# Kernel optimization log

Hardware: AMD Instinct MI355X
Metric: run time of the kernel (lower is better)

## Reference

```python
import jax, jax.numpy as jnp
import numpy as np

EPS = 1e-7  # K.epsilon()


def setup_inputs() -> dict:
    key = jax.random.key(0)
    k1, k2, k3, k4 = jax.random.split(key, 4)
    B, T, S = 512, 32, 2048  # batch, time_steps, seq_len
    inputs = jax.random.normal(k1, (B, T, S), dtype=jnp.float32)
    # Keras mask (float 0/1), same shape as inputs
    mask = (jax.random.uniform(k2, (B, T, S)) < 0.8).astype(jnp.float32)
    # 'uniform' keras initializer: U(-0.05, 0.05)
    W = jax.random.uniform(k3, (S, T, T), minval=-0.05, maxval=0.05, dtype=jnp.float32)
    b = jax.random.uniform(k4, (S, T), minval=-0.05, maxval=0.05, dtype=jnp.float32)
    return {"inputs": inputs, "mask": mask, "W": W, "b": b}


def reference(inputs, mask, W, b):
    # (B,T,S) -> (B,S,T), apply mask
    x = jnp.transpose(inputs, (0, 2, 1)) * jnp.transpose(mask, (0, 2, 1))
    # per-position matmul, batched over B and S (replaces the tf.scan over batch)
    z = jnp.einsum('bst,stu->bsu', x, W) + b  # (B,S,T)
    e = jnp.exp(jnp.tanh(z))
    att = e / (jnp.sum(e, axis=2, keepdims=True) + EPS)  # softmax-like over T
    return jnp.sum(att * x, axis=1)  # (B,T)
```

## Files before the change

kernel.cpp:

```cpp
#include <hip/hip_runtime.h>

#define EPS_K 1e-7f

typedef __attribute__((ext_vector_type(8)))  short          frag8;
typedef __attribute__((ext_vector_type(16))) float          accf16;
typedef __attribute__((ext_vector_type(4)))  unsigned short us4;

__device__ __forceinline__ unsigned f2bf(float f) {
  union { float f; unsigned u; } v; v.f = f;
  unsigned u = v.u;
  u += 0x7FFFu + ((u >> 16) & 1u);
  return u >> 16;
}
__device__ __forceinline__ float bf2f(unsigned short s) {
  union { unsigned u; float f; } v; v.u = ((unsigned)s) << 16;
  return v.f;
}
__device__ __forceinline__ unsigned pk_bf16(float lo, float hi) {
  return f2bf(lo) | (f2bf(hi) << 16);
}

__global__ __launch_bounds__(256) void wbf_prep(
    const float* __restrict__ Wt, unsigned short* __restrict__ Wbf)
{
  __shared__ unsigned short tile[32 * 33];
  const int s   = blockIdx.x;
  const int tid = threadIdx.x;
  {
    const int t  = tid >> 3;
    const int uc = tid & 7;
    const float4 v = *(const float4*)(Wt + s * 1024 + t * 32 + 4 * uc);
    tile[t * 33 + 4 * uc + 0] = (unsigned short)f2bf(v.x);
    tile[t * 33 + 4 * uc + 1] = (unsigned short)f2bf(v.y);
    tile[t * 33 + 4 * uc + 2] = (unsigned short)f2bf(v.z);
    tile[t * 33 + 4 * uc + 3] = (unsigned short)f2bf(v.w);
  }
  __syncthreads();
  {
    const int u  = tid >> 3;
    const int tc = tid & 7;
    uint2 d;
    d.x = (unsigned)tile[(4 * tc + 0) * 33 + u] | ((unsigned)tile[(4 * tc + 1) * 33 + u] << 16);
    d.y = (unsigned)tile[(4 * tc + 2) * 33 + u] | ((unsigned)tile[(4 * tc + 3) * 33 + u] << 16);
    *(uint2*)(Wbf + s * 1024 + u * 32 + 4 * tc) = d;
  }
}

template <bool WBF>
__global__ __launch_bounds__(256, 5) void attn_fused(
    const float* __restrict__ inp,
    const float* __restrict__ msk,
    const float* __restrict__ Wt,
    const unsigned short* __restrict__ Wbf,
    const float* __restrict__ bias,
    float* __restrict__ out)
{
  __shared__ unsigned short x_us[32 * 256];

  const int tid = threadIdx.x;
  const int st  = blockIdx.x >> 4;
  const int bg  = blockIdx.x & 15;
  const int s0  = st * 8;

  {
    const int sc = tid & 1;
    const int tb = (tid >> 1) & 3;
    const int b  = tid >> 3;
    const float* ip = inp + ((size_t)(bg * 32 + b) * 32 + 8 * tb) * 2048 + s0 + 4 * sc;
    const float* mp = msk + ((size_t)(bg * 32 + b) * 32 + 8 * tb) * 2048 + s0 + 4 * sc;
    unsigned c32[4][4];
    #pragma unroll
    for (int j2 = 0; j2 < 4; ++j2) {
      const float4 vi0 = *(const float4*)(ip + (2 * j2)     * 2048);
      const float4 vm0 = *(const float4*)(mp + (2 * j2)     * 2048);
      const float4 vi1 = *(const float4*)(ip + (2 * j2 + 1) * 2048);
      const float4 vm1 = *(const float4*)(mp + (2 * j2 + 1) * 2048);
      c32[0][j2] = pk_bf16(vi0.x * vm0.x, vi1.x * vm1.x);
      c32[1][j2] = pk_bf16(vi0.y * vm0.y, vi1.y * vm1.y);
      c32[2][j2] = pk_bf16(vi0.z * vm0.z, vi1.z * vm1.z);
      c32[3][j2] = pk_bf16(vi0.w * vm0.w, vi1.w * vm1.w);
    }
    #pragma unroll
    for (int w = 0; w < 4; ++w) {
      const int L = tb * 8 + 4 * sc + w;
      unsigned* dst = (unsigned*)(x_us + b * 256 + ((L ^ (b & 7)) * 8));
      *(uint4*)dst = make_uint4(c32[w][0], c32[w][1], c32[w][2], c32[w][3]);
    }
  }
  __syncthreads();

  const int lane = tid & 63;
  const int wv   = tid >> 6;
  const int n    = lane & 31;
  const int h    = lane >> 5;
  const int nx   = n & 7;

  float O[16];
  #pragma unroll
  for (int r = 0; r < 16; ++r) O[r] = 0.f;

  #pragma unroll
  for (int si = 0; si < 2; ++si) {
    const int sl = wv * 2 + si;
    const int s  = s0 + sl;

    frag8 a1, a2;
    if (WBF) {
      const unsigned short* wp = Wbf + s * 1024 + n * 32 + 8 * h;
      a1 = *(const frag8*)(wp);
      a2 = *(const frag8*)(wp + 16);
    } else {
      const float* Wp = Wt + s * 1024;
      #pragma unroll
      for (int j = 0; j < 8; ++j) {
        const int t1 = 8 * h + j;
        a1[j] = (short)f2bf(Wp[t1 * 32 + n]);
        a2[j] = (short)f2bf(Wp[(t1 + 16) * 32 + n]);
      }
    }

    const frag8 b1 = *(const frag8*)(x_us + n * 256 + (((h      * 8 + sl) ^ nx) * 8));
    const frag8 b2 = *(const frag8*)(x_us + n * 256 + ((((h + 2) * 8 + sl) ^ nx) * 8));

    accf16 acc;
    #pragma unroll
    for (int g = 0; g < 4; ++g) {
      const float4 bb = *(const float4*)(bias + s * 32 + 8 * g + 4 * h);
      acc[4 * g + 0] = bb.x; acc[4 * g + 1] = bb.y;
      acc[4 * g + 2] = bb.z; acc[4 * g + 3] = bb.w;
    }
    acc = __builtin_amdgcn_mfma_f32_32x32x16_bf16(a1, b1, acc, 0, 0, 0);
    acc = __builtin_amdgcn_mfma_f32_32x32x16_bf16(a2, b2, acc, 0, 0, 0);

    float ps = 0.f;
    #pragma unroll
    for (int r = 0; r < 16; ++r) {
      const float z  = acc[r];
      const float e2 = __expf(2.f * z);
      const float th = 1.f - 2.f / (e2 + 1.f);
      acc[r] = __expf(th);
      ps    += acc[r];
    }
    const float tot = ps + __shfl_xor(ps, 32, 64);
    const float inv = 1.f / (tot + EPS_K);

    #pragma unroll
    for (int g = 0; g < 4; ++g) {
      const us4 xv = *(const us4*)(x_us + n * 256 + (((g * 8 + sl) ^ nx) * 8) + 4 * h);
      #pragma unroll
      for (int i = 0; i < 4; ++i)
        O[4 * g + i] += acc[4 * g + i] * inv * bf2f(xv[i]);
    }
  }

  __syncthreads();
  float* red = (float*)x_us;
  #pragma unroll
  for (int r = 0; r < 16; ++r) {
    const int u = (r & 3) + 8 * (r >> 2) + 4 * h;
    red[wv * 1024 + n * 32 + (u ^ n)] = O[r];
  }
  __syncthreads();

  const int q0 = tid * 4;
  #pragma unroll
  for (int i = 0; i < 4; ++i) {
    const int q = q0 + i;
    const int b = q >> 5, u = q & 31;
    float sum = 0.f;
    #pragma unroll
    for (int w = 0; w < 4; ++w) sum += red[w * 1024 + b * 32 + (u ^ b)];
    atomicAdd(out + bg * 1024 + q, sum);
  }
}

extern "C" void kernel_launch(void* const* d_in, const int* in_sizes, int n_in,
                              void* d_out, int out_size, void* d_ws, size_t ws_size,
                              hipStream_t stream) {
  const float* inp  = (const float*)d_in[0];
  const float* msk  = (const float*)d_in[1];
  const float* Wt   = (const float*)d_in[2];
  const float* bias = (const float*)d_in[3];
  float* out = (float*)d_out;

  const size_t wbf_sz = (size_t)2048 * 1024 * sizeof(unsigned short);

  (void)hipMemsetAsync(out, 0, (size_t)out_size * sizeof(float), stream);

  if (ws_size >= wbf_sz) {
    unsigned short* Wbf = (unsigned short*)d_ws;
    wbf_prep<<<dim3(2048), dim3(256), 0, stream>>>(Wt, Wbf);
    attn_fused<true><<<dim3(4096), dim3(256), 0, stream>>>(
        inp, msk, Wt, Wbf, bias, out);
  } else {
    attn_fused<false><<<dim3(4096), dim3(256), 0, stream>>>(
        inp, msk, Wt, nullptr, bias, out);
  }
}
```

Measured before the change: 322.2 us.

## Split into repack, MFMA compute and deterministic reduction kernels

Adds a separate pass that reads inputs and mask with coalesced wide loads and writes a masked bf16 copy in a swizzled per-batch-group layout. The compute kernel then reads that layout directly and processes 32 positions per block. It writes partial sums to a workspace, which a final kernel reduces, replacing atomics and the memset. Reciprocals now use the hardware rcp instruction. The cost is an extra bf16 write and read of the activations plus two more launches, and a slow naive fallback runs when the workspace is too small.

```diff
diff --git a/kernel.cpp b/kernel.cpp
--- a/kernel.cpp
+++ b/kernel.cpp
@@ -5,6 +5,7 @@
 typedef __attribute__((ext_vector_type(8)))  short          frag8;
 typedef __attribute__((ext_vector_type(16))) float          accf16;
 typedef __attribute__((ext_vector_type(4)))  unsigned short us4;
+typedef __attribute__((ext_vector_type(4)))  float          f32x4;
 
 __device__ __forceinline__ unsigned f2bf(float f) {
   union { float f; unsigned u; } v; v.f = f;
@@ -16,8 +17,8 @@
   union { unsigned u; float f; } v; v.u = ((unsigned)s) << 16;
   return v.f;
 }
-__device__ __forceinline__ unsigned pk_bf16(float lo, float hi) {
-  return f2bf(lo) | (f2bf(hi) << 16);
+__device__ __forceinline__ float rcp_f(float x) {
+  return __builtin_amdgcn_rcpf(x);
 }
 
 __global__ __launch_bounds__(256) void wbf_prep(
@@ -46,88 +47,91 @@
   }
 }
 
-template <bool WBF>
-__global__ __launch_bounds__(256, 5) void attn_fused(
-    const float* __restrict__ inp,
-    const float* __restrict__ msk,
-    const float* __restrict__ Wt,
+__global__ __launch_bounds__(512, 4) void repack(
+    const float* __restrict__ inp, const float* __restrict__ msk,
+    unsigned short* __restrict__ Y)
+{
+  __shared__ unsigned short sl[32768];
+  const int tid  = threadIdx.x;
+  const int lane = tid & 63;
+  const int b7   = tid >> 6;
+  const int Q    = blockIdx.x & 63;
+  const int w    = blockIdx.x >> 6;
+  const int l5   = lane >> 5;
+  const int l31  = lane & 31;
+
+  const size_t rbase = ((size_t)(Q * 8 + b7) * 32 + l5) * 2048 + w * 128 + 4 * l31;
+  const int xb = (b7 ^ (lane & 7)) * 8;
+
+  #pragma unroll
+  for (int p0 = 0; p0 < 16; p0 += 4) {
+    f32x4 vi[4], vm[4];
+    #pragma unroll
+    for (int q = 0; q < 4; ++q) {
+      const size_t off = rbase + (size_t)(2 * (p0 + q)) * 2048;
+      vi[q] = *(const f32x4*)(inp + off);
+      vm[q] = *(const f32x4*)(msk + off);
+    }
+    #pragma unroll
+    for (int q = 0; q < 4; ++q) {
+      const int t_ = 2 * (p0 + q) + l5;
+      const int ab = (t_ >> 3) * 64 + (t_ & 7) + xb;
+      #pragma unroll
+      for (int k = 0; k < 4; ++k)
+        sl[(4 * l31 + k) * 256 + ab] = (unsigned short)f2bf(vi[q][k] * vm[q][k]);
+    }
+  }
+  __syncthreads();
+
+  const size_t ybyte = ((size_t)Q * 2048 + (size_t)w * 128) * 512;
+  #pragma unroll
+  for (int i = 0; i < 8; ++i) {
+    const int e = i * 512 + tid;
+    const uint4 d = *(const uint4*)((const char*)sl + (size_t)e * 16);
+    *(uint4*)((char*)Y + ybyte + (size_t)e * 16) = d;
+  }
+}
+
+__global__ __launch_bounds__(256, 4) void attn_comp(
+    const unsigned short* __restrict__ Y,
     const unsigned short* __restrict__ Wbf,
     const float* __restrict__ bias,
-    float* __restrict__ out)
-{
-  __shared__ unsigned short x_us[32 * 256];
-
-  const int tid = threadIdx.x;
-  const int st  = blockIdx.x >> 4;
-  const int bg  = blockIdx.x & 15;
-  const int s0  = st * 8;
-
-  {
-    const int sc = tid & 1;
-    const int tb = (tid >> 1) & 3;
-    const int b  = tid >> 3;
-    const float* ip = inp + ((size_t)(bg * 32 + b) * 32 + 8 * tb) * 2048 + s0 + 4 * sc;
-    const float* mp = msk + ((size_t)(bg * 32 + b) * 32 + 8 * tb) * 2048 + s0 + 4 * sc;
-    unsigned c32[4][4];
-    #pragma unroll
-    for (int j2 = 0; j2 < 4; ++j2) {
-      const float4 vi0 = *(const float4*)(ip + (2 * j2)     * 2048);
-      const float4 vm0 = *(const float4*)(mp + (2 * j2)     * 2048);
-      const float4 vi1 = *(const float4*)(ip + (2 * j2 + 1) * 2048);
-      const float4 vm1 = *(const float4*)(mp + (2 * j2 + 1) * 2048);
-      c32[0][j2] = pk_bf16(vi0.x * vm0.x, vi1.x * vm1.x);
-      c32[1][j2] = pk_bf16(vi0.y * vm0.y, vi1.y * vm1.y);
-      c32[2][j2] = pk_bf16(vi0.z * vm0.z, vi1.z * vm1.z);
-      c32[3][j2] = pk_bf16(vi0.w * vm0.w, vi1.w * vm1.w);
-    }
-    #pragma unroll
-    for (int w = 0; w < 4; ++w) {
-      const int L = tb * 8 + 4 * sc + w;
-      unsigned* dst = (unsigned*)(x_us + b * 256 + ((L ^ (b & 7)) * 8));
-      *(uint4*)dst = make_uint4(c32[w][0], c32[w][1], c32[w][2], c32[w][3]);
-    }
-  }
-  __syncthreads();
-
+    float* __restrict__ part)
+{
+  __shared__ float red[4096];
+  const int tid  = threadIdx.x;
+  const int bg   = blockIdx.x & 15;
+  const int sg   = blockIdx.x >> 4;
   const int lane = tid & 63;
   const int wv   = tid >> 6;
   const int n    = lane & 31;
   const int h    = lane >> 5;
-  const int nx   = n & 7;
+
+  const unsigned short* Yq = Y + ((size_t)(bg * 4 + (n >> 3)) * 2048) * 256;
 
   float O[16];
   #pragma unroll
   for (int r = 0; r < 16; ++r) O[r] = 0.f;
 
-  #pragma unroll
-  for (int si = 0; si < 2; ++si) {
-    const int sl = wv * 2 + si;
-    const int s  = s0 + sl;
-
-    frag8 a1, a2;
-    if (WBF) {
-      const unsigned short* wp = Wbf + s * 1024 + n * 32 + 8 * h;
-      a1 = *(const frag8*)(wp);
-      a2 = *(const frag8*)(wp + 16);
-    } else {
-      const float* Wp = Wt + s * 1024;
-      #pragma unroll
-      for (int j = 0; j < 8; ++j) {
-        const int t1 = 8 * h + j;
-        a1[j] = (short)f2bf(Wp[t1 * 32 + n]);
-        a2[j] = (short)f2bf(Wp[(t1 + 16) * 32 + n]);
-      }
-    }
-
-    const frag8 b1 = *(const frag8*)(x_us + n * 256 + (((h      * 8 + sl) ^ nx) * 8));
-    const frag8 b2 = *(const frag8*)(x_us + n * 256 + ((((h + 2) * 8 + sl) ^ nx) * 8));
+  #pragma unroll 2
+  for (int it = 0; it < 8; ++it) {
+    const int s = sg * 32 + wv * 8 + it;
+    const unsigned short* slp = Yq + (size_t)s * 256;
+    const int bt = (((n & 7) ^ ((s >> 2) & 7)) * 8);
+
+    const frag8 b1 = *(const frag8*)(slp + h * 64 + bt);
+    const frag8 b2 = *(const frag8*)(slp + (h + 2) * 64 + bt);
+
+    const unsigned short* wp = Wbf + (size_t)s * 1024 + n * 32 + 8 * h;
+    const frag8 a1 = *(const frag8*)(wp);
+    const frag8 a2 = *(const frag8*)(wp + 16);
 
     accf16 acc;
     #pragma unroll
     for (int g = 0; g < 4; ++g) {
-      const float4 bb = *(const float4*)(bias + s * 32 + 8 * g + 4 * h);
-      acc[4 * g + 0] = bb.x; acc[4 * g + 1] = bb.y;
-      acc[4 * g + 2] = bb.z; acc[4 * g + 3] = bb.w;
+      const f32x4 bb = *(const f32x4*)(bias + s * 32 + 8 * g + 4 * h);
+      acc[4 * g + 0] = bb[0]; acc[4 * g + 1] = bb[1];
+      acc[4 * g + 2] = bb[2]; acc[4 * g + 3] = bb[3];
     }
     acc = __builtin_amdgcn_mfma_f32_32x32x16_bf16(a1, b1, acc, 0, 0, 0);
     acc = __builtin_amdgcn_mfma_f32_32x32x16_bf16(a2, b2, acc, 0, 0, 0);
@@ -137,24 +141,22 @@
     for (int r = 0; r < 16; ++r) {
       const float z  = acc[r];
       const float e2 = __expf(2.f * z);
-      const float th = 1.f - 2.f / (e2 + 1.f);
+      const float th = 1.f - 2.f * rcp_f(e2 + 1.f);
       acc[r] = __expf(th);
       ps    += acc[r];
     }
     const float tot = ps + __shfl_xor(ps, 32, 64);
-    const float inv = 1.f / (tot + EPS_K);
+    const float inv = rcp_f(tot + EPS_K);
 
     #pragma unroll
     for (int g = 0; g < 4; ++g) {
-      const us4 xv = *(const us4*)(x_us + n * 256 + (((g * 8 + sl) ^ nx) * 8) + 4 * h);
+      const us4 xv = *(const us4*)(slp + g * 64 + bt + 4 * h);
       #pragma unroll
       for (int i = 0; i < 4; ++i)
         O[4 * g + i] += acc[4 * g + i] * inv * bf2f(xv[i]);
     }
   }
 
-  __syncthreads();
-  float* red = (float*)x_us;
   #pragma unroll
   for (int r = 0; r < 16; ++r) {
     const int u = (r & 3) + 8 * (r >> 2) + 4 * h;
@@ -163,6 +165,7 @@
   __syncthreads();
 
   const int q0 = tid * 4;
+  f32x4 v;
   #pragma unroll
   for (int i = 0; i < 4; ++i) {
     const int q = q0 + i;
@@ -170,8 +173,48 @@
     float sum = 0.f;
     #pragma unroll
     for (int w = 0; w < 4; ++w) sum += red[w * 1024 + b * 32 + (u ^ b)];
-    atomicAdd(out + bg * 1024 + q, sum);
-  }
+    v[i] = sum;
+  }
+  *(f32x4*)(part + (size_t)sg * 16384 + bg * 1024 + q0) = v;
+}
+
+__global__ __launch_bounds__(256) void reduce_part(
+    const float* __restrict__ part, float* __restrict__ out)
+{
+  const int f = blockIdx.x * 256 + threadIdx.x;
+  float s = 0.f;
+  #pragma unroll 8
+  for (int sg = 0; sg < 64; ++sg) s += part[(size_t)sg * 16384 + f];
+  out[f] = s;
+}
+
+__global__ __launch_bounds__(256) void attn_naive(
+    const float* __restrict__ inp, const float* __restrict__ msk,
+    const float* __restrict__ Wt, const float* __restrict__ bias,
+    float* __restrict__ out)
+{
+  const int idx = blockIdx.x * 256 + threadIdx.x;
+  const int b = idx >> 5, sc = idx & 31;
+  float O[32];
+  #pragma unroll
+  for (int u = 0; u < 32; ++u) O[u] = 0.f;
+  for (int si = 0; si < 64; ++si) {
+    const int s = sc * 64 + si;
+    float x[32], z[32];
+    for (int t = 0; t < 32; ++t) {
+      x[t] = inp[((size_t)b * 32 + t) * 2048 + s] * msk[((size_t)b * 32 + t) * 2048 + s];
+      z[t] = bias[s * 32 + t];
+    }
+    for (int t = 0; t < 32; ++t) {
+      const float xv = x[t];
+      for (int u = 0; u < 32; ++u) z[u] += xv * Wt[(size_t)s * 1024 + t * 32 + u];
+    }
+    float e[32], ps = 0.f;
+    for (int u = 0; u < 32; ++u) { e[u] = expf(tanhf(z[u])); ps += e[u]; }
+    const float inv = 1.f / (ps + EPS_K);
+    for (int u = 0; u < 32; ++u) O[u] += e[u] * inv * x[u];
+  }
+  for (int u = 0; u < 32; ++u) atomicAdd(out + b * 32 + u, O[u]);
 }
 
 extern "C" void kernel_launch(void* const* d_in, const int* in_sizes, int n_in,
@@ -183,17 +226,20 @@
   const float* bias = (const float*)d_in[3];
   float* out = (float*)d_out;
 
-  const size_t wbf_sz = (size_t)2048 * 1024 * sizeof(unsigned short);
-
-  (void)hipMemsetAsync(out, 0, (size_t)out_size * sizeof(float), stream);
-
-  if (ws_size >= wbf_sz) {
-    unsigned short* Wbf = (unsigned short*)d_ws;
+  const size_t part_sz = (size_t)64 * 16384 * sizeof(float);
+  const size_t wbf_sz  = (size_t)2048 * 1024 * sizeof(unsigned short);
+  const size_t y_sz    = (size_t)512 * 32 * 2048 * sizeof(unsigned short);
+
+  if (ws_size >= part_sz + wbf_sz + y_sz) {
+    float* part = (float*)d_ws;
+    unsigned short* Wbf = (unsigned short*)((char*)d_ws + part_sz);
+    unsigned short* Y   = (unsigned short*)((char*)d_ws + part_sz + wbf_sz);
+    repack<<<dim3(1024), dim3(512), 0, stream>>>(inp, msk, Y);
     wbf_prep<<<dim3(2048), dim3(256), 0, stream>>>(Wt, Wbf);
-    attn_fused<true><<<dim3(4096), dim3(256), 0, stream>>>(
-        inp, msk, Wt, Wbf, bias, out);
+    attn_comp<<<dim3(1024), dim3(256), 0, stream>>>(Y, Wbf, bias, part);
+    reduce_part<<<dim3(64), dim3(256), 0, stream>>>(part, out);
   } else {
-    attn_fused<false><<<dim3(4096), dim3(256), 0, stream>>>(
-        inp, msk, Wt, nullptr, bias, out);
-  }
-}
+    (void)hipMemsetAsync(out, 0, (size_t)out_size * sizeof(float), stream);
+    attn_naive<<<dim3(64), dim3(256), 0, stream>>>(inp, msk, Wt, bias, out);
+  }
+}
```

After: 333.9 us. +3.6%, slower.
